# Optimization experiments

Hardware: AMD Instinct MI355X
Metric: run time of the kernel (lower is better)

## Reference

```python
import jax, jax.numpy as jnp
import numpy as np

L, B, E = 2048, 4, 1024
H = 8
D1 = 2048          # expand_ratio * E, multiple of H
HD = D1 // H       # head dim 256
MAX_L = 2048
EPS = 1e-8


def setup_inputs() -> dict:
    key = jax.random.key(0)
    ks = jax.random.split(key, 9)
    std = 0.02
    return {
        "x": jax.random.normal(ks[0], (L, B, E), jnp.float32),
        "Wu": jax.random.normal(ks[1], (D1, E), jnp.float32) * std,
        "bu": jax.random.normal(ks[2], (D1,), jnp.float32) * std,
        "Wv": jax.random.normal(ks[3], (D1, E), jnp.float32) * std,
        "bv": jax.random.normal(ks[4], (D1,), jnp.float32) * std,
        "Wo": jax.random.normal(ks[5], (E, D1), jnp.float32) * std,
        "bo": jax.random.normal(ks[6], (E,), jnp.float32) * std,
        "zero": jax.random.normal(ks[7], (H, 1), jnp.float32) * 0.1,   # Toeplitz coef, offset 0
        "pos": jax.random.normal(ks[8], (H, MAX_L - 1), jnp.float32) * 0.1,  # offsets 1..n-1
    }


def _simple_rmsnorm(x):
    d = x.shape[-1]
    rms = jnp.linalg.norm(x, axis=-1, keepdims=True) * (d ** -0.5)
    return x / (rms + EPS)


def _toeplitz_causal_fft(v, zero, pos):
    # v: (b, h, n, hd); causal Toeplitz mixing along n via FFT long conv
    n = v.shape[-2]
    coef = jnp.concatenate([zero, pos[:, : n - 1]], axis=-1)  # (h, n)
    m = 2 * n
    cf = jnp.fft.rfft(coef, m, axis=-1)                  # (h, m//2+1)
    vf = jnp.fft.rfft(v, m, axis=-2)                     # (b, h, m//2+1, hd)
    out = jnp.fft.irfft(cf[None, :, :, None] * vf, m, axis=-2)
    return out[:, :, :n, :]


def reference(x, Wu, bu, Wv, bv, Wo, bo, zero, pos):
    # x: (n, b, e) fairseq layout
    n, b, e = x.shape
    shortcut = x
    xn = _simple_rmsnorm(x)                               # pre_norm (SimpleRMSNorm, no params)
    u = jax.nn.silu(jnp.einsum('nbe,de->nbd', xn, Wu) + bu)   # (n,b,d1)
    v = jax.nn.silu(jnp.einsum('nbe,de->nbd', xn, Wv) + bv)   # (n,b,d1)
    # 'n b (h d) -> b h n d'
    vh = v.transpose(1, 0, 2).reshape(b, n, H, HD).transpose(0, 2, 1, 3)
    oh = _toeplitz_causal_fft(vh, zero, pos)              # (b,h,n,hd)
    o = oh.transpose(0, 2, 1, 3).reshape(b, n, D1).transpose(1, 0, 2)  # (n,b,d1)
    o = u * o                                             # gating
    out = jnp.einsum('nbd,ed->nbe', o, Wo) + bo + shortcut
    return out
```

## Files before the change

### kernel.cpp

```cpp
#include <hip/hip_runtime.h>
#include <cstdint>
#include <cstddef>

#define LQ   2048
#define BQ   4
#define EQ   1024
#define HQ   8
#define D1Q  2048
#define HDQ  256
#define NBQ  (LQ*BQ)

typedef __bf16 bf16_t;
typedef __bf16 bf16x8 __attribute__((ext_vector_type(8)));
typedef __bf16 bf16x4 __attribute__((ext_vector_type(4)));
typedef float  f32x4  __attribute__((ext_vector_type(4)));

#define GAS1(p) ((const __attribute__((address_space(1))) void*)(p))
#define LAS3(p) ((__attribute__((address_space(3))) void*)(p))


__global__ __launch_bounds__(256) void convert_kernel(
    const float* __restrict__ Wu, const float* __restrict__ Wv,
    const float* __restrict__ Wo,
    bf16_t* __restrict__ Wub, bf16_t* __restrict__ Wvb,
    bf16_t* __restrict__ Wob)
{
    const size_t i = (size_t)blockIdx.x * 256 + threadIdx.x;
    if (i < (size_t)D1Q * EQ) {
        Wub[i] = (bf16_t)Wu[i];
        Wvb[i] = (bf16_t)Wv[i];
        Wob[i] = (bf16_t)Wo[i];
    }
}

__global__ __launch_bounds__(256) void build_toep_tiles(
    const float* __restrict__ zero, const float* __restrict__ pos,
    bf16_t* __restrict__ Atiles)
{
    const int q = blockIdx.x;
    const int h = blockIdx.y;
    const int doff = (q - 3) * 32;
    const int tid = threadIdx.x;
    bf16_t* dst = Atiles + ((size_t)h * 64 + q) * (128 * 32);
    const int e0 = tid * 16;
    const int r = e0 >> 5;
    const int cbase = e0 & 31;
    bf16_t vals[16];
    #pragma unroll
    for (int j = 0; j < 16; ++j) {
        const int d = doff + r - (cbase + j);
        float v = 0.f;
        if (d == 0) v = zero[h];
        else if (d > 0) v = pos[(size_t)h * (LQ - 1) + d - 1];
        vals[j] = (bf16_t)v;
    }
    *(bf16x8*)(dst + e0)     = *(bf16x8*)(vals);
    *(bf16x8*)(dst + e0 + 8) = *(bf16x8*)(vals + 8);
}

__global__ __launch_bounds__(256) void rmsnorm_kernel(
    const float* __restrict__ x, bf16_t* __restrict__ xn)
{
    const int row = blockIdx.x;
    const int tid = threadIdx.x;
    const float4 v = ((const float4*)(x + (size_t)row * EQ))[tid];
    float ss = v.x*v.x + v.y*v.y + v.z*v.z + v.w*v.w;
    #pragma unroll
    for (int m = 32; m >= 1; m >>= 1) ss += __shfl_xor(ss, m, 64);
    __shared__ float red[4];
    const int wid = tid >> 6, lane = tid & 63;
    if (lane == 0) red[wid] = ss;
    __syncthreads();
    const float tot = red[0] + red[1] + red[2] + red[3];
    const float inv = 1.f / (sqrtf(tot * (1.f / EQ)) + 1e-8f);
    bf16x4 o;
    o[0] = (bf16_t)(v.x * inv); o[1] = (bf16_t)(v.y * inv);
    o[2] = (bf16_t)(v.z * inv); o[3] = (bf16_t)(v.w * inv);
    *(bf16x4*)(xn + (size_t)row * EQ + tid * 4) = o;
}

__global__ __launch_bounds__(512, 4) void gemm_uv(
    const bf16_t* __restrict__ A, const bf16_t* __restrict__ Bm,
    const float* __restrict__ bbu, const float* __restrict__ bbv,
    bf16_t* __restrict__ Ub, bf16_t* __restrict__ Vt)
{
    constexpr int K = EQ;
    constexpr int BUF = 24576;
    __shared__ alignas(16) char smem[2 * BUF];

    const int nwg   = gridDim.x * gridDim.y;
    const int bid0  = blockIdx.y * gridDim.x + blockIdx.x;
    const int chunkw = nwg >> 3;
    const int sb    = (bid0 & 7) * chunkw + (bid0 >> 3);
    const int bx    = sb % gridDim.x;
    const int by    = sb / gridDim.x;

    const int tid  = threadIdx.x;
    const int wid  = tid >> 6;
    const int lane = tid & 63;
    const int frow = lane & 15;
    const int c    = lane >> 4;
    const int m0 = by * 256;
    const int n0 = bx * 128;
    const int wm = wid >> 1, wn = wid & 1;
    const int wrm = wm * 64, wrn = wn * 64;

    const int g = (frow >> 1) & 3;
    const int offA0 = (wrm + frow) * 64 + ((c ^ g) << 4);
    const int offB0 = 16384 + (wrn + frow) * 64 + ((c ^ g) << 4);

    const int rA   = tid >> 2;
    const int soff = (((tid & 3) ^ ((rA >> 1) & 3)) << 4);
    const size_t lda2 = (size_t)K * 2;
    const char* sA = (const char*)A  + (size_t)(m0 + rA) * lda2 + soff;
    const char* sB = (const char*)Bm + (size_t)(n0 + rA) * lda2 + soff;

    auto STAGE = [&](int bf, int kt) {
        char* dA = smem + bf * BUF + wid * 1024;
        __builtin_amdgcn_global_load_lds(GAS1(sA + (size_t)kt * 64), LAS3(dA), 16, 0, 0);
        __builtin_amdgcn_global_load_lds(GAS1(sA + 128 * lda2 + (size_t)kt * 64),
                                         LAS3(dA + 8192), 16, 0, 0);
        char* dB = smem + bf * BUF + 16384 + wid * 1024;
        __builtin_amdgcn_global_load_lds(GAS1(sB + (size_t)kt * 64), LAS3(dB), 16, 0, 0);
    };

    f32x4 acc[4][4];
    #pragma unroll
    for (int i = 0; i < 4; ++i)
        #pragma unroll
        for (int j = 0; j < 4; ++j) acc[i][j] = (f32x4){0.f, 0.f, 0.f, 0.f};

    const int NT = K >> 5;

    STAGE(0, 0);
    asm volatile("s_waitcnt vmcnt(0)" ::: "memory");
    __builtin_amdgcn_s_barrier();

    for (int t = 0; t < NT; ++t) {
        if (t + 1 < NT) STAGE((t + 1) & 1, t + 1);
        const char* base = smem + (t & 1) * BUF;
        bf16x8 av[4], bv[4];
        #pragma unroll
        for (int i = 0; i < 4; ++i) {
            av[i] = *(const bf16x8*)(base + offA0 + i * 1024);
            bv[i] = *(const bf16x8*)(base + offB0 + i * 1024);
        }
        __builtin_amdgcn_s_setprio(1);
        #pragma unroll
        for (int mi = 0; mi < 4; ++mi)
            #pragma unroll
            for (int ni = 0; ni < 4; ++ni)
                acc[mi][ni] = __builtin_amdgcn_mfma_f32_16x16x32_bf16(
                    av[mi], bv[ni], acc[mi][ni], 0, 0, 0);
        __builtin_amdgcn_s_setprio(0);
        asm volatile("s_waitcnt vmcnt(0)" ::: "memory");
        __builtin_amdgcn_s_barrier();
    }

    if (bx < 16) {
        const int fq = c * 4;
        #pragma unroll
        for (int mi = 0; mi < 4; ++mi) {
            #pragma unroll
            for (int ni = 0; ni < 4; ++ni) {
                const int gn = n0 + wrn + ni * 16 + frow;
                #pragma unroll
                for (int j = 0; j < 4; ++j) {
                    const int gm = m0 + wrm + mi * 16 + fq + j;
                    float v = acc[mi][ni][j] + bbu[gn];
                    v = v / (1.f + __expf(-v));
                    Ub[(size_t)gm * D1Q + gn] = (bf16_t)v;
                }
            }
        }
        return;
    }

    {
        const int n0v = n0 - 2048;
        const int hh  = n0v >> 8;
        const int hdb = (n0v & 255) + wrn;
        float bb[4];
        #pragma unroll
        for (int ni = 0; ni < 4; ++ni) bb[ni] = bbv[n0v + wrn + ni * 16 + frow];

        bf16_t* chunk = (bf16_t*)smem + wn * 8448;
        #pragma unroll
        for (int p = 0; p < 2; ++p) {
            __syncthreads();
            #pragma unroll
            for (int mi = 0; mi < 4; ++mi) {
                #pragma unroll
                for (int nio = 0; nio < 2; ++nio) {
                    const int ni = p * 2 + nio;
                    const int nl = nio * 16 + frow;
                    const int tl = wm * 16 + mi * 4 + c;
                    #pragma unroll
                    for (int j = 0; j < 4; ++j) {
                        float v = acc[mi][ni][j] + bb[ni];
                        v = v / (1.f + __expf(-v));
                        chunk[nl * 264 + j * 64 + tl] = (bf16_t)v;
                    }
                }
            }
            __syncthreads();
            const int nl    = lane & 31;
            const int thalf = lane >> 5;
            const int b2    = wm;
            const int hd    = hdb + p * 32 + nl;
            const int t0    = (m0 >> 2) + thalf * 32;
            const bf16_t* src = chunk + nl * 264 + b2 * 64 + thalf * 32;
            bf16_t* dst = Vt + (((size_t)hh * 4 + b2) * 256 + hd) * (size_t)LQ + t0;
            #pragma unroll
            for (int u = 0; u < 4; ++u)
                *(bf16x8*)(dst + u * 8) = *(const bf16x8*)(src + u * 8);
        }
    }
}

__global__ __launch_bounds__(256, 4) void gemm_toep(
    const bf16_t* __restrict__ VT, const bf16_t* __restrict__ Atiles,
    const bf16_t* __restrict__ U, bf16_t* __restrict__ O)
{
    constexpr int BUF = 16384;
    __shared__ alignas(16) char smem[2 * BUF];

    const int bid   = blockIdx.x;
    const int m_blk = 15 - (bid >> 6);
    const int sub   = bid & 63;
    const int h     = sub >> 3;
    const int n0    = (sub & 7) * 128;
    const int m0    = m_blk * 128;

    const int tid  = threadIdx.x;
    const int wid  = tid >> 6;
    const int lane = tid & 63;
    const int frow = lane & 15;
    const int c    = lane >> 4;
    const int wm = wid >> 1, wn = wid & 1;
    const int wrm = wm * 64, wrn = wn * 64;

    const int g = (frow >> 1) & 3;
    const int offA0 = (wrm + frow) * 64 + ((c ^ g) << 4);
    const int offB0 = 8192 + (wrn + frow) * 64 + ((c ^ g) << 4);

    const int rA   = tid >> 2;
    const int soff = (((tid & 3) ^ ((rA >> 1) & 3)) << 4);
    const char* Ah = (const char*)Atiles + (size_t)h * 64 * 8192;
    const size_t ldb = (size_t)LQ * 2;
    const char* sB = (const char*)VT + ((size_t)h * 1024 + n0 + rA) * ldb + soff;

    auto STAGE = [&](int bf, int kt) {
        const int q = 4 * m_blk + 3 - kt;
        const char* s = Ah + (size_t)q * 8192 + (size_t)rA * 64 + soff;
        char* dA = smem + bf * BUF + wid * 1024;
        __builtin_amdgcn_global_load_lds(GAS1(s), LAS3(dA), 16, 0, 0);
        __builtin_amdgcn_global_load_lds(GAS1(s + 4096), LAS3(dA + 4096), 16, 0, 0);
        char* dB = smem + bf * BUF + 8192 + wid * 1024;
        __builtin_amdgcn_global_load_lds(GAS1(sB + (size_t)kt * 64), LAS3(dB), 16, 0, 0);
        __builtin_amdgcn_global_load_lds(GAS1(sB + 64 * ldb + (size_t)kt * 64),
                                         LAS3(dB + 4096), 16, 0, 0);
    };

    f32x4 acc[4][4];
    #pragma unroll
    for (int i = 0; i < 4; ++i)
        #pragma unroll
        for (int j = 0; j < 4; ++j) acc[i][j] = (f32x4){0.f, 0.f, 0.f, 0.f};

    const int NT = 4 * m_blk + 4;

    STAGE(0, 0);
    asm volatile("s_waitcnt vmcnt(0)" ::: "memory");
    __builtin_amdgcn_s_barrier();

    for (int t = 0; t < NT; ++t) {
        if (t + 1 < NT) STAGE((t + 1) & 1, t + 1);
        const char* base = smem + (t & 1) * BUF;
        bf16x8 av[4], bv[4];
        #pragma unroll
        for (int i = 0; i < 4; ++i) {
            av[i] = *(const bf16x8*)(base + offA0 + i * 1024);
            bv[i] = *(const bf16x8*)(base + offB0 + i * 1024);
        }
        __builtin_amdgcn_s_setprio(1);
        #pragma unroll
        for (int mi = 0; mi < 4; ++mi)
            #pragma unroll
            for (int ni = 0; ni < 4; ++ni)
                acc[mi][ni] = __builtin_amdgcn_mfma_f32_16x16x32_bf16(
                    av[mi], bv[ni], acc[mi][ni], 0, 0, 0);
        __builtin_amdgcn_s_setprio(0);
        asm volatile("s_waitcnt vmcnt(0)" ::: "memory");
        __builtin_amdgcn_s_barrier();
    }

    const int fq = c * 4;
    #pragma unroll
    for (int mi = 0; mi < 4; ++mi) {
        #pragma unroll
        for (int ni = 0; ni < 4; ++ni) {
            const int nn = n0 + wrn + ni * 16 + frow;
            const int b  = nn >> 8, hd = nn & 255;
            #pragma unroll
            for (int j = 0; j < 4; ++j) {
                const int t = m0 + wrm + mi * 16 + fq + j;
                const size_t idx = ((size_t)t * BQ + b) * D1Q + h * HDQ + hd;
                const float uval = (float)U[idx];
                O[idx] = (bf16_t)(uval * acc[mi][ni][j]);
            }
        }
    }
}

__global__ __launch_bounds__(256, 4) void gemm_fin(
    const bf16_t* __restrict__ A, const bf16_t* __restrict__ Bm,
    const float* __restrict__ bias, const float* __restrict__ res,
    float* __restrict__ Cf)
{
    constexpr int K = D1Q, N = EQ;
    constexpr int BUF = 16384;
    __shared__ alignas(16) char smem[2 * BUF];

    const int nwg   = gridDim.x * gridDim.y;
    const int bid0  = blockIdx.y * gridDim.x + blockIdx.x;
    const int chunkw = nwg >> 3;
    const int sb    = (bid0 & 7) * chunkw + (bid0 >> 3);
    const int bx    = sb % gridDim.x;
    const int by    = sb / gridDim.x;

    const int tid  = threadIdx.x;
    const int wid  = tid >> 6;
    const int lane = tid & 63;
    const int frow = lane & 15;
    const int c    = lane >> 4;
    const int m0 = by * 128;
    const int n0 = bx * 128;
    const int wm = wid >> 1, wn = wid & 1;
    const int wrm = wm * 64, wrn = wn * 64;

    const int g = (frow >> 1) & 3;
    const int offA0 = (wrm + frow) * 64 + ((c ^ g) << 4);
    const int offB0 = 8192 + (wrn + frow) * 64 + ((c ^ g) << 4);

    const int rA   = tid >> 2;
    const int soff = (((tid & 3) ^ ((rA >> 1) & 3)) << 4);
    const size_t lda2 = (size_t)K * 2;
    const char* sA = (const char*)A  + (size_t)(m0 + rA) * lda2 + soff;
    const char* sB = (const char*)Bm + (size_t)(n0 + rA) * lda2 + soff;

    auto STAGE = [&](int bf, int kt) {
        char* dA = smem + bf * BUF + wid * 1024;
        __builtin_amdgcn_global_load_lds(GAS1(sA + (size_t)kt * 64), LAS3(dA), 16, 0, 0);
        __builtin_amdgcn_global_load_lds(GAS1(sA + 64 * lda2 + (size_t)kt * 64),
                                         LAS3(dA + 4096), 16, 0, 0);
        char* dB = smem + bf * BUF + 8192 + wid * 1024;
        __builtin_amdgcn_global_load_lds(GAS1(sB + (size_t)kt * 64), LAS3(dB), 16, 0, 0);
        __builtin_amdgcn_global_load_lds(GAS1(sB + 64 * lda2 + (size_t)kt * 64),
                                         LAS3(dB + 4096), 16, 0, 0);
    };

    f32x4 acc[4][4];
    #pragma unroll
    for (int i = 0; i < 4; ++i)
        #pragma unroll
        for (int j = 0; j < 4; ++j) acc[i][j] = (f32x4){0.f, 0.f, 0.f, 0.f};

    const int NT = K >> 5;

    STAGE(0, 0);
    asm volatile("s_waitcnt vmcnt(0)" ::: "memory");
    __builtin_amdgcn_s_barrier();

    for (int t = 0; t < NT; ++t) {
        if (t + 1 < NT) STAGE((t + 1) & 1, t + 1);
        const char* base = smem + (t & 1) * BUF;
        bf16x8 av[4], bv[4];
        #pragma unroll
        for (int i = 0; i < 4; ++i) {
            av[i] = *(const bf16x8*)(base + offA0 + i * 1024);
            bv[i] = *(const bf16x8*)(base + offB0 + i * 1024);
        }
        __builtin_amdgcn_s_setprio(1);
        #pragma unroll
        for (int mi = 0; mi < 4; ++mi)
            #pragma unroll
            for (int ni = 0; ni < 4; ++ni)
                acc[mi][ni] = __builtin_amdgcn_mfma_f32_16x16x32_bf16(
                    av[mi], bv[ni], acc[mi][ni], 0, 0, 0);
        __builtin_amdgcn_s_setprio(0);
        asm volatile("s_waitcnt vmcnt(0)" ::: "memory");
        __builtin_amdgcn_s_barrier();
    }

    const int fq = c * 4;
    #pragma unroll
    for (int mi = 0; mi < 4; ++mi) {
        #pragma unroll
        for (int ni = 0; ni < 4; ++ni) {
            const int gn = n0 + wrn + ni * 16 + frow;
            #pragma unroll
            for (int j = 0; j < 4; ++j) {
                const int gm = m0 + wrm + mi * 16 + fq + j;
                Cf[(size_t)gm * N + gn] =
                    acc[mi][ni][j] + bias[gn] + res[(size_t)gm * N + gn];
            }
        }
    }
}


extern "C" void kernel_launch(void* const* d_in, const int* in_sizes, int n_in,
                              void* d_out, int out_size, void* d_ws, size_t ws_size,
                              hipStream_t stream)
{
    const float* x    = (const float*)d_in[0];
    const float* Wu   = (const float*)d_in[1];
    const float* bu   = (const float*)d_in[2];
    const float* Wv   = (const float*)d_in[3];
    const float* bv   = (const float*)d_in[4];
    const float* Wo   = (const float*)d_in[5];
    const float* bo   = (const float*)d_in[6];
    const float* zero = (const float*)d_in[7];
    const float* pos  = (const float*)d_in[8];
    float* out = (float*)d_out;

    char* ws = (char*)d_ws;
    size_t off = 0;
    auto alloc = [&](size_t bytes) {
        char* p = ws + off;
        off += (bytes + 255) & ~(size_t)255;
        return p;
    };
    bf16_t* xn     = (bf16_t*)alloc((size_t)NBQ * EQ * 2);
    bf16_t* Wub    = (bf16_t*)alloc((size_t)D1Q * EQ * 2);
    bf16_t* Wvb    = (bf16_t*)alloc((size_t)D1Q * EQ * 2);
    bf16_t* Wob    = (bf16_t*)alloc((size_t)EQ * D1Q * 2);
    bf16_t* Atiles = (bf16_t*)alloc((size_t)HQ * 64 * 4096 * 2);
    bf16_t* Ub     = (bf16_t*)alloc((size_t)NBQ * D1Q * 2);
    bf16_t* VTb    = (bf16_t*)alloc((size_t)NBQ * D1Q * 2);
    bf16_t* Ob     = (bf16_t*)alloc((size_t)NBQ * D1Q * 2);

    convert_kernel<<<8192, 256, 0, stream>>>(Wu, Wv, Wo, Wub, Wvb, Wob);
    build_toep_tiles<<<dim3(64, 8), 256, 0, stream>>>(zero, pos, Atiles);
    rmsnorm_kernel<<<NBQ, 256, 0, stream>>>(x, xn);

    dim3 g1(32, NBQ / 256);
    gemm_uv<<<g1, 512, 0, stream>>>(xn, Wub, bu, bv, Ub, VTb);

    gemm_toep<<<1024, 256, 0, stream>>>(VTb, Atiles, Ub, Ob);

    dim3 g2(EQ / 128, NBQ / 128);
    gemm_fin<<<g2, 256, 0, stream>>>(Ob, Wob, bo, x, out);
}
```

Before: 200.2 us.

## Triple-buffer LDS staging in all GEMMs and shrink gemm_uv tile to 128x128

All three GEMM kernels move from double to triple LDS buffering, prefetching two k-tiles ahead and waiting only on the older batch of loads (vmcnt(4)), so global loads overlap compute more deeply. gemm_uv also moves from 512-thread 256x128 tiles to 256-thread 128x128 tiles, and its transposed V write-back epilogue is rewritten to match. The added LDS per block lowers the occupancy hints from 4 to 3 blocks per CU, which may reduce latency hiding across waves.

```diff
diff --git a/kernel.cpp b/kernel.cpp
--- a/kernel.cpp
+++ b/kernel.cpp
@@ -79,14 +79,15 @@
     *(bf16x4*)(xn + (size_t)row * EQ + tid * 4) = o;
 }
 
-__global__ __launch_bounds__(512, 4) void gemm_uv(
+
+__global__ __launch_bounds__(256, 3) void gemm_uv(
     const bf16_t* __restrict__ A, const bf16_t* __restrict__ Bm,
     const float* __restrict__ bbu, const float* __restrict__ bbv,
     bf16_t* __restrict__ Ub, bf16_t* __restrict__ Vt)
 {
     constexpr int K = EQ;
-    constexpr int BUF = 24576;
-    __shared__ alignas(16) char smem[2 * BUF];
+    constexpr int BUF = 16384;
+    __shared__ alignas(16) char smem[3 * BUF];
 
     const int nwg   = gridDim.x * gridDim.y;
     const int bid0  = blockIdx.y * gridDim.x + blockIdx.x;
@@ -100,14 +101,14 @@
     const int lane = tid & 63;
     const int frow = lane & 15;
     const int c    = lane >> 4;
-    const int m0 = by * 256;
+    const int m0 = by * 128;
     const int n0 = bx * 128;
     const int wm = wid >> 1, wn = wid & 1;
     const int wrm = wm * 64, wrn = wn * 64;
 
     const int g = (frow >> 1) & 3;
     const int offA0 = (wrm + frow) * 64 + ((c ^ g) << 4);
-    const int offB0 = 16384 + (wrn + frow) * 64 + ((c ^ g) << 4);
+    const int offB0 = 8192 + (wrn + frow) * 64 + ((c ^ g) << 4);
 
     const int rA   = tid >> 2;
     const int soff = (((tid & 3) ^ ((rA >> 1) & 3)) << 4);
@@ -118,10 +119,12 @@
     auto STAGE = [&](int bf, int kt) {
         char* dA = smem + bf * BUF + wid * 1024;
         __builtin_amdgcn_global_load_lds(GAS1(sA + (size_t)kt * 64), LAS3(dA), 16, 0, 0);
-        __builtin_amdgcn_global_load_lds(GAS1(sA + 128 * lda2 + (size_t)kt * 64),
-                                         LAS3(dA + 8192), 16, 0, 0);
-        char* dB = smem + bf * BUF + 16384 + wid * 1024;
+        __builtin_amdgcn_global_load_lds(GAS1(sA + 64 * lda2 + (size_t)kt * 64),
+                                         LAS3(dA + 4096), 16, 0, 0);
+        char* dB = smem + bf * BUF + 8192 + wid * 1024;
         __builtin_amdgcn_global_load_lds(GAS1(sB + (size_t)kt * 64), LAS3(dB), 16, 0, 0);
+        __builtin_amdgcn_global_load_lds(GAS1(sB + 64 * lda2 + (size_t)kt * 64),
+                                         LAS3(dB + 4096), 16, 0, 0);
     };
 
     f32x4 acc[4][4];
@@ -132,13 +135,14 @@
 
     const int NT = K >> 5;
 
-    STAGE(0, 0);
-    asm volatile("s_waitcnt vmcnt(0)" ::: "memory");
+    STAGE(0, 0); STAGE(1, 1);
+    asm volatile("s_waitcnt vmcnt(4)" ::: "memory");
     __builtin_amdgcn_s_barrier();
 
+    int cur = 0, pb = 2;
     for (int t = 0; t < NT; ++t) {
-        if (t + 1 < NT) STAGE((t + 1) & 1, t + 1);
-        const char* base = smem + (t & 1) * BUF;
+        if (t + 2 < NT) STAGE(pb, t + 2);
+        const char* base = smem + cur * BUF;
         bf16x8 av[4], bv[4];
         #pragma unroll
         for (int i = 0; i < 4; ++i) {
@@ -153,8 +157,13 @@
                 acc[mi][ni] = __builtin_amdgcn_mfma_f32_16x16x32_bf16(
                     av[mi], bv[ni], acc[mi][ni], 0, 0, 0);
         __builtin_amdgcn_s_setprio(0);
-        asm volatile("s_waitcnt vmcnt(0)" ::: "memory");
-        __builtin_amdgcn_s_barrier();
+        if (t + 1 < NT) {
+            if (t + 2 < NT) asm volatile("s_waitcnt vmcnt(4)" ::: "memory");
+            else            asm volatile("s_waitcnt vmcnt(0)" ::: "memory");
+            __builtin_amdgcn_s_barrier();
+        }
+        cur = (cur == 2) ? 0 : cur + 1;
+        pb  = (pb  == 2) ? 0 : pb  + 1;
     }
 
     if (bx < 16) {
@@ -177,40 +186,40 @@
     }
 
     {
-        const int n0v = n0 - 2048;
-        const int hh  = n0v >> 8;
-        const int hdb = (n0v & 255) + wrn;
+        const int bxv = bx - 16;
+        const int hh  = bxv >> 1;
+        const int hd0 = (bxv & 1) * 128;
+        const int n0v = bxv * 128;
         float bb[4];
         #pragma unroll
         for (int ni = 0; ni < 4; ++ni) bb[ni] = bbv[n0v + wrn + ni * 16 + frow];
 
-        bf16_t* chunk = (bf16_t*)smem + wn * 8448;
-        #pragma unroll
-        for (int p = 0; p < 2; ++p) {
-            __syncthreads();
-            #pragma unroll
-            for (int mi = 0; mi < 4; ++mi) {
+        __syncthreads();
+        bf16_t* chunk = (bf16_t*)smem;
+        const int tl0 = wm * 16 + c;
+        #pragma unroll
+        for (int mi = 0; mi < 4; ++mi) {
+            #pragma unroll
+            for (int ni = 0; ni < 4; ++ni) {
+                const int hdl = wrn + ni * 16 + frow;
                 #pragma unroll
-                for (int nio = 0; nio < 2; ++nio) {
-                    const int ni = p * 2 + nio;
-                    const int nl = nio * 16 + frow;
-                    const int tl = wm * 16 + mi * 4 + c;
-                    #pragma unroll
-                    for (int j = 0; j < 4; ++j) {
-                        float v = acc[mi][ni][j] + bb[ni];
-                        v = v / (1.f + __expf(-v));
-                        chunk[nl * 264 + j * 64 + tl] = (bf16_t)v;
-                    }
+                for (int j = 0; j < 4; ++j) {
+                    float v = acc[mi][ni][j] + bb[ni];
+                    v = v / (1.f + __expf(-v));
+                    chunk[hdl * 136 + j * 32 + tl0 + mi * 4] = (bf16_t)v;
                 }
             }
-            __syncthreads();
-            const int nl    = lane & 31;
-            const int thalf = lane >> 5;
-            const int b2    = wm;
-            const int hd    = hdb + p * 32 + nl;
-            const int t0    = (m0 >> 2) + thalf * 32;
-            const bf16_t* src = chunk + nl * 264 + b2 * 64 + thalf * 32;
-            bf16_t* dst = Vt + (((size_t)hh * 4 + b2) * 256 + hd) * (size_t)LQ + t0;
+        }
+        __syncthreads();
+        const int nl  = lane & 31;
+        const int bs  = lane >> 5;
+        const int hdl = wid * 32 + nl;
+        const int t0  = m0 >> 2;
+        #pragma unroll
+        for (int bi = 0; bi < 2; ++bi) {
+            const int b2 = bs * 2 + bi;
+            const bf16_t* src = chunk + hdl * 136 + b2 * 32;
+            bf16_t* dst = Vt + (((size_t)hh * 4 + b2) * 256 + hd0 + hdl) * (size_t)LQ + t0;
             #pragma unroll
             for (int u = 0; u < 4; ++u)
                 *(bf16x8*)(dst + u * 8) = *(const bf16x8*)(src + u * 8);
@@ -218,12 +227,12 @@
     }
 }
 
-__global__ __launch_bounds__(256, 4) void gemm_toep(
+__global__ __launch_bounds__(256, 3) void gemm_toep(
     const bf16_t* __restrict__ VT, const bf16_t* __restrict__ Atiles,
     const bf16_t* __restrict__ U, bf16_t* __restrict__ O)
 {
     constexpr int BUF = 16384;
-    __shared__ alignas(16) char smem[2 * BUF];
+    __shared__ alignas(16) char smem[3 * BUF];
 
     const int bid   = blockIdx.x;
     const int m_blk = 15 - (bid >> 6);
@@ -270,13 +279,14 @@
 
     const int NT = 4 * m_blk + 4;
 
-    STAGE(0, 0);
-    asm volatile("s_waitcnt vmcnt(0)" ::: "memory");
+    STAGE(0, 0); STAGE(1, 1);
+    asm volatile("s_waitcnt vmcnt(4)" ::: "memory");
     __builtin_amdgcn_s_barrier();
 
+    int cur = 0, pb = 2;
     for (int t = 0; t < NT; ++t) {
-        if (t + 1 < NT) STAGE((t + 1) & 1, t + 1);
-        const char* base = smem + (t & 1) * BUF;
+        if (t + 2 < NT) STAGE(pb, t + 2);
+        const char* base = smem + cur * BUF;
         bf16x8 av[4], bv[4];
         #pragma unroll
         for (int i = 0; i < 4; ++i) {
@@ -291,8 +301,13 @@
                 acc[mi][ni] = __builtin_amdgcn_mfma_f32_16x16x32_bf16(
                     av[mi], bv[ni], acc[mi][ni], 0, 0, 0);
         __builtin_amdgcn_s_setprio(0);
-        asm volatile("s_waitcnt vmcnt(0)" ::: "memory");
-        __builtin_amdgcn_s_barrier();
+        if (t + 1 < NT) {
+            if (t + 2 < NT) asm volatile("s_waitcnt vmcnt(4)" ::: "memory");
+            else            asm volatile("s_waitcnt vmcnt(0)" ::: "memory");
+            __builtin_amdgcn_s_barrier();
+        }
+        cur = (cur == 2) ? 0 : cur + 1;
+        pb  = (pb  == 2) ? 0 : pb  + 1;
     }
 
     const int fq = c * 4;
@@ -313,14 +328,14 @@
     }
 }
 
-__global__ __launch_bounds__(256, 4) void gemm_fin(
+__global__ __launch_bounds__(256, 3) void gemm_fin(
     const bf16_t* __restrict__ A, const bf16_t* __restrict__ Bm,
     const float* __restrict__ bias, const float* __restrict__ res,
     float* __restrict__ Cf)
 {
     constexpr int K = D1Q, N = EQ;
     constexpr int BUF = 16384;
-    __shared__ alignas(16) char smem[2 * BUF];
+    __shared__ alignas(16) char smem[3 * BUF];
 
     const int nwg   = gridDim.x * gridDim.y;
     const int bid0  = blockIdx.y * gridDim.x + blockIdx.x;
@@ -368,13 +383,14 @@
 
     const int NT = K >> 5;
 
-    STAGE(0, 0);
-    asm volatile("s_waitcnt vmcnt(0)" ::: "memory");
+    STAGE(0, 0); STAGE(1, 1);
+    asm volatile("s_waitcnt vmcnt(4)" ::: "memory");
     __builtin_amdgcn_s_barrier();
 
+    int cur = 0, pb = 2;
     for (int t = 0; t < NT; ++t) {
-        if (t + 1 < NT) STAGE((t + 1) & 1, t + 1);
-        const char* base = smem + (t & 1) * BUF;
+        if (t + 2 < NT) STAGE(pb, t + 2);
+        const char* base = smem + cur * BUF;
         bf16x8 av[4], bv[4];
         #pragma unroll
         for (int i = 0; i < 4; ++i) {
@@ -389,8 +405,13 @@
                 acc[mi][ni] = __builtin_amdgcn_mfma_f32_16x16x32_bf16(
                     av[mi], bv[ni], acc[mi][ni], 0, 0, 0);
         __builtin_amdgcn_s_setprio(0);
-        asm volatile("s_waitcnt vmcnt(0)" ::: "memory");
-        __builtin_amdgcn_s_barrier();
+        if (t + 1 < NT) {
+            if (t + 2 < NT) asm volatile("s_waitcnt vmcnt(4)" ::: "memory");
+            else            asm volatile("s_waitcnt vmcnt(0)" ::: "memory");
+            __builtin_amdgcn_s_barrier();
+        }
+        cur = (cur == 2) ? 0 : cur + 1;
+        pb  = (pb  == 2) ? 0 : pb  + 1;
     }
 
     const int fq = c * 4;
@@ -445,8 +466,8 @@
     build_toep_tiles<<<dim3(64, 8), 256, 0, stream>>>(zero, pos, Atiles);
     rmsnorm_kernel<<<NBQ, 256, 0, stream>>>(x, xn);
 
-    dim3 g1(32, NBQ / 256);
-    gemm_uv<<<g1, 512, 0, stream>>>(xn, Wub, bu, bv, Ub, VTb);
+    dim3 g1(32, NBQ / 128);
+    gemm_uv<<<g1, 256, 0, stream>>>(xn, Wub, bu, bv, Ub, VTb);
 
     gemm_toep<<<1024, 256, 0, stream>>>(VTb, Atiles, Ub, Ob);
 
```

After: 216.9 us. 1.08x slower.

## Load B operands directly from global into registers, bypassing LDS in GEMMs

Applied to the files above, without the earlier changes.

All three GEMMs now read their B-operand fragments straight from global memory into registers each k-step, and only the A tile is staged through LDS. This shrinks LDS buffers and cuts LDS traffic. The Toeplitz GEMM is retiled to 512-thread blocks covering 256 columns, which halves the grid, and the weight conversion kernel is vectorised to float4. The cost is that B loads are uncoalesced per-lane 16-byte reads issued inside the loop with no prefetch, so global latency may be exposed; launch bounds and occupancy change as well.

```diff
diff --git a/kernel.cpp b/kernel.cpp
--- a/kernel.cpp
+++ b/kernel.cpp
@@ -25,11 +25,18 @@
     bf16_t* __restrict__ Wub, bf16_t* __restrict__ Wvb,
     bf16_t* __restrict__ Wob)
 {
-    const size_t i = (size_t)blockIdx.x * 256 + threadIdx.x;
+    const size_t i = ((size_t)blockIdx.x * 256 + threadIdx.x) * 4;
     if (i < (size_t)D1Q * EQ) {
-        Wub[i] = (bf16_t)Wu[i];
-        Wvb[i] = (bf16_t)Wv[i];
-        Wob[i] = (bf16_t)Wo[i];
+        float4 a = *(const float4*)(Wu + i);
+        float4 b = *(const float4*)(Wv + i);
+        float4 d = *(const float4*)(Wo + i);
+        bf16x4 oa, ob, od;
+        oa[0]=(bf16_t)a.x; oa[1]=(bf16_t)a.y; oa[2]=(bf16_t)a.z; oa[3]=(bf16_t)a.w;
+        ob[0]=(bf16_t)b.x; ob[1]=(bf16_t)b.y; ob[2]=(bf16_t)b.z; ob[3]=(bf16_t)b.w;
+        od[0]=(bf16_t)d.x; od[1]=(bf16_t)d.y; od[2]=(bf16_t)d.z; od[3]=(bf16_t)d.w;
+        *(bf16x4*)(Wub + i) = oa;
+        *(bf16x4*)(Wvb + i) = ob;
+        *(bf16x4*)(Wob + i) = od;
     }
 }
 
@@ -79,14 +86,15 @@
     *(bf16x4*)(xn + (size_t)row * EQ + tid * 4) = o;
 }
 
-__global__ __launch_bounds__(512, 4) void gemm_uv(
+
+__global__ __launch_bounds__(512, 2) void gemm_uv(
     const bf16_t* __restrict__ A, const bf16_t* __restrict__ Bm,
     const float* __restrict__ bbu, const float* __restrict__ bbv,
     bf16_t* __restrict__ Ub, bf16_t* __restrict__ Vt)
 {
     constexpr int K = EQ;
-    constexpr int BUF = 24576;
-    __shared__ alignas(16) char smem[2 * BUF];
+    constexpr int BUF = 16384;
+    __shared__ alignas(16) char smem[36864];
 
     const int nwg   = gridDim.x * gridDim.y;
     const int bid0  = blockIdx.y * gridDim.x + blockIdx.x;
@@ -107,21 +115,22 @@
 
     const int g = (frow >> 1) & 3;
     const int offA0 = (wrm + frow) * 64 + ((c ^ g) << 4);
-    const int offB0 = 16384 + (wrn + frow) * 64 + ((c ^ g) << 4);
 
     const int rA   = tid >> 2;
     const int soff = (((tid & 3) ^ ((rA >> 1) & 3)) << 4);
     const size_t lda2 = (size_t)K * 2;
-    const char* sA = (const char*)A  + (size_t)(m0 + rA) * lda2 + soff;
-    const char* sB = (const char*)Bm + (size_t)(n0 + rA) * lda2 + soff;
+    const char* sA = (const char*)A + (size_t)(m0 + rA) * lda2 + soff;
+
+    const bf16_t* bp[4];
+    #pragma unroll
+    for (int ni = 0; ni < 4; ++ni)
+        bp[ni] = Bm + (size_t)(n0 + wrn + ni * 16 + frow) * K + c * 8;
 
     auto STAGE = [&](int bf, int kt) {
         char* dA = smem + bf * BUF + wid * 1024;
         __builtin_amdgcn_global_load_lds(GAS1(sA + (size_t)kt * 64), LAS3(dA), 16, 0, 0);
         __builtin_amdgcn_global_load_lds(GAS1(sA + 128 * lda2 + (size_t)kt * 64),
                                          LAS3(dA + 8192), 16, 0, 0);
-        char* dB = smem + bf * BUF + 16384 + wid * 1024;
-        __builtin_amdgcn_global_load_lds(GAS1(sB + (size_t)kt * 64), LAS3(dB), 16, 0, 0);
     };
 
     f32x4 acc[4][4];
@@ -137,14 +146,16 @@
     __builtin_amdgcn_s_barrier();
 
     for (int t = 0; t < NT; ++t) {
+        bf16x8 bv[4];
+        #pragma unroll
+        for (int ni = 0; ni < 4; ++ni)
+            bv[ni] = *(const bf16x8*)(bp[ni] + t * 32);
         if (t + 1 < NT) STAGE((t + 1) & 1, t + 1);
         const char* base = smem + (t & 1) * BUF;
-        bf16x8 av[4], bv[4];
-        #pragma unroll
-        for (int i = 0; i < 4; ++i) {
+        bf16x8 av[4];
+        #pragma unroll
+        for (int i = 0; i < 4; ++i)
             av[i] = *(const bf16x8*)(base + offA0 + i * 1024);
-            bv[i] = *(const bf16x8*)(base + offB0 + i * 1024);
-        }
         __builtin_amdgcn_s_setprio(1);
         #pragma unroll
         for (int mi = 0; mi < 4; ++mi)
@@ -218,18 +229,18 @@
     }
 }
 
-__global__ __launch_bounds__(256, 4) void gemm_toep(
+__global__ __launch_bounds__(512, 2) void gemm_toep(
     const bf16_t* __restrict__ VT, const bf16_t* __restrict__ Atiles,
     const bf16_t* __restrict__ U, bf16_t* __restrict__ O)
 {
-    constexpr int BUF = 16384;
+    constexpr int BUF = 8192;
     __shared__ alignas(16) char smem[2 * BUF];
 
     const int bid   = blockIdx.x;
-    const int m_blk = 15 - (bid >> 6);
-    const int sub   = bid & 63;
-    const int h     = sub >> 3;
-    const int n0    = (sub & 7) * 128;
+    const int m_blk = 15 - (bid >> 5);
+    const int sub   = bid & 31;
+    const int h     = sub >> 2;
+    const int n0    = (sub & 3) * 256;
     const int m0    = m_blk * 128;
 
     const int tid  = threadIdx.x;
@@ -237,29 +248,26 @@
     const int lane = tid & 63;
     const int frow = lane & 15;
     const int c    = lane >> 4;
-    const int wm = wid >> 1, wn = wid & 1;
-    const int wrm = wm * 64, wrn = wn * 64;
+    const int wrm  = (wid >> 2) * 64;
+    const int wrn  = (wid & 3) * 64;
 
     const int g = (frow >> 1) & 3;
     const int offA0 = (wrm + frow) * 64 + ((c ^ g) << 4);
-    const int offB0 = 8192 + (wrn + frow) * 64 + ((c ^ g) << 4);
 
     const int rA   = tid >> 2;
     const int soff = (((tid & 3) ^ ((rA >> 1) & 3)) << 4);
     const char* Ah = (const char*)Atiles + (size_t)h * 64 * 8192;
-    const size_t ldb = (size_t)LQ * 2;
-    const char* sB = (const char*)VT + ((size_t)h * 1024 + n0 + rA) * ldb + soff;
+
+    const bf16_t* bp[4];
+    #pragma unroll
+    for (int ni = 0; ni < 4; ++ni)
+        bp[ni] = VT + ((size_t)h * 1024 + n0 + wrn + ni * 16 + frow) * LQ + c * 8;
 
     auto STAGE = [&](int bf, int kt) {
         const int q = 4 * m_blk + 3 - kt;
         const char* s = Ah + (size_t)q * 8192 + (size_t)rA * 64 + soff;
-        char* dA = smem + bf * BUF + wid * 1024;
-        __builtin_amdgcn_global_load_lds(GAS1(s), LAS3(dA), 16, 0, 0);
-        __builtin_amdgcn_global_load_lds(GAS1(s + 4096), LAS3(dA + 4096), 16, 0, 0);
-        char* dB = smem + bf * BUF + 8192 + wid * 1024;
-        __builtin_amdgcn_global_load_lds(GAS1(sB + (size_t)kt * 64), LAS3(dB), 16, 0, 0);
-        __builtin_amdgcn_global_load_lds(GAS1(sB + 64 * ldb + (size_t)kt * 64),
-                                         LAS3(dB + 4096), 16, 0, 0);
+        __builtin_amdgcn_global_load_lds(GAS1(s),
+                                         LAS3(smem + bf * BUF + wid * 1024), 16, 0, 0);
     };
 
     f32x4 acc[4][4];
@@ -275,14 +283,16 @@
     __builtin_amdgcn_s_barrier();
 
     for (int t = 0; t < NT; ++t) {
+        bf16x8 bv[4];
+        #pragma unroll
+        for (int ni = 0; ni < 4; ++ni)
+            bv[ni] = *(const bf16x8*)(bp[ni] + t * 32);
         if (t + 1 < NT) STAGE((t + 1) & 1, t + 1);
         const char* base = smem + (t & 1) * BUF;
-        bf16x8 av[4], bv[4];
-        #pragma unroll
-        for (int i = 0; i < 4; ++i) {
+        bf16x8 av[4];
+        #pragma unroll
+        for (int i = 0; i < 4; ++i)
             av[i] = *(const bf16x8*)(base + offA0 + i * 1024);
-            bv[i] = *(const bf16x8*)(base + offB0 + i * 1024);
-        }
         __builtin_amdgcn_s_setprio(1);
         #pragma unroll
         for (int mi = 0; mi < 4; ++mi)
@@ -313,13 +323,13 @@
     }
 }
 
-__global__ __launch_bounds__(256, 4) void gemm_fin(
+__global__ __launch_bounds__(256, 3) void gemm_fin(
     const bf16_t* __restrict__ A, const bf16_t* __restrict__ Bm,
     const float* __restrict__ bias, const float* __restrict__ res,
     float* __restrict__ Cf)
 {
     constexpr int K = D1Q, N = EQ;
-    constexpr int BUF = 16384;
+    constexpr int BUF = 8192;
     __shared__ alignas(16) char smem[2 * BUF];
 
     const int nwg   = gridDim.x * gridDim.y;
@@ -341,23 +351,22 @@
 
     const int g = (frow >> 1) & 3;
     const int offA0 = (wrm + frow) * 64 + ((c ^ g) << 4);
-    const int offB0 = 8192 + (wrn + frow) * 64 + ((c ^ g) << 4);
 
     const int rA   = tid >> 2;
     const int soff = (((tid & 3) ^ ((rA >> 1) & 3)) << 4);
     const size_t lda2 = (size_t)K * 2;
-    const char* sA = (const char*)A  + (size_t)(m0 + rA) * lda2 + soff;
-    const char* sB = (const char*)Bm + (size_t)(n0 + rA) * lda2 + soff;
+    const char* sA = (const char*)A + (size_t)(m0 + rA) * lda2 + soff;
+
+    const bf16_t* bp[4];
+    #pragma unroll
+    for (int ni = 0; ni < 4; ++ni)
+        bp[ni] = Bm + (size_t)(n0 + wrn + ni * 16 + frow) * K + c * 8;
 
     auto STAGE = [&](int bf, int kt) {
         char* dA = smem + bf * BUF + wid * 1024;
         __builtin_amdgcn_global_load_lds(GAS1(sA + (size_t)kt * 64), LAS3(dA), 16, 0, 0);
         __builtin_amdgcn_global_load_lds(GAS1(sA + 64 * lda2 + (size_t)kt * 64),
                                          LAS3(dA + 4096), 16, 0, 0);
-        char* dB = smem + bf * BUF + 8192 + wid * 1024;
-        __builtin_amdgcn_global_load_lds(GAS1(sB + (size_t)kt * 64), LAS3(dB), 16, 0, 0);
-        __builtin_amdgcn_global_load_lds(GAS1(sB + 64 * lda2 + (size_t)kt * 64),
-                                         LAS3(dB + 4096), 16, 0, 0);
     };
 
     f32x4 acc[4][4];
@@ -373,14 +382,16 @@
     __builtin_amdgcn_s_barrier();
 
     for (int t = 0; t < NT; ++t) {
+        bf16x8 bv[4];
+        #pragma unroll
+        for (int ni = 0; ni < 4; ++ni)
+            bv[ni] = *(const bf16x8*)(bp[ni] + t * 32);
         if (t + 1 < NT) STAGE((t + 1) & 1, t + 1);
         const char* base = smem + (t & 1) * BUF;
-        bf16x8 av[4], bv[4];
-        #pragma unroll
-        for (int i = 0; i < 4; ++i) {
+        bf16x8 av[4];
+        #pragma unroll
+        for (int i = 0; i < 4; ++i)
             av[i] = *(const bf16x8*)(base + offA0 + i * 1024);
-            bv[i] = *(const bf16x8*)(base + offB0 + i * 1024);
-        }
         __builtin_amdgcn_s_setprio(1);
         #pragma unroll
         for (int mi = 0; mi < 4; ++mi)
@@ -441,14 +452,14 @@
     bf16_t* VTb    = (bf16_t*)alloc((size_t)NBQ * D1Q * 2);
     bf16_t* Ob     = (bf16_t*)alloc((size_t)NBQ * D1Q * 2);
 
-    convert_kernel<<<8192, 256, 0, stream>>>(Wu, Wv, Wo, Wub, Wvb, Wob);
+    convert_kernel<<<2048, 256, 0, stream>>>(Wu, Wv, Wo, Wub, Wvb, Wob);
     build_toep_tiles<<<dim3(64, 8), 256, 0, stream>>>(zero, pos, Atiles);
     rmsnorm_kernel<<<NBQ, 256, 0, stream>>>(x, xn);
 
     dim3 g1(32, NBQ / 256);
     gemm_uv<<<g1, 512, 0, stream>>>(xn, Wub, bu, bv, Ub, VTb);
 
-    gemm_toep<<<1024, 256, 0, stream>>>(VTb, Atiles, Ub, Ob);
+    gemm_toep<<<512, 512, 0, stream>>>(VTb, Atiles, Ub, Ob);
 
     dim3 g2(EQ / 128, NBQ / 128);
     gemm_fin<<<g2, 256, 0, stream>>>(Ob, Wob, bo, x, out);
```

New measurement: 365.2 us. 1.82x slower.
